# Optimization experiments

Hardware: AMD Instinct MI355X
Metric: run time of the kernel (lower is better)

The kernel has to match this reference:

```python
import jax, jax.numpy as jnp
import numpy as np

H = 128        # num_hidden
NIN = 384      # num_in
FF = 4 * H
SCALE = 30.0
EPS = 1e-5


def _gelu(x):
    return jax.nn.gelu(x, approximate=False)


def _layernorm(x, g, b):
    mu = jnp.mean(x, axis=-1, keepdims=True)
    var = jnp.var(x, axis=-1, keepdims=True)
    return (x - mu) * jax.lax.rsqrt(var + EPS) * g + b


def setup_inputs() -> dict:
    key = jax.random.key(0)
    ks = jax.random.split(key, 12)
    B, N, K = 4, 2048, 48
    s = lambda fan_in: 1.0 / np.sqrt(fan_in)
    inp = {
        "h_V": jax.random.normal(ks[0], (B, N, H), jnp.float32),
        "h_E": jax.random.normal(ks[1], (B, N, K, NIN), jnp.float32),
        "mask_V": jnp.ones((B, N), jnp.float32),
        "mask_attend": jnp.ones((B, N, K), jnp.float32),
        "W1_w": jax.random.uniform(ks[2], (H + NIN, H), jnp.float32, -s(H + NIN), s(H + NIN)),
        "W1_b": jnp.zeros((H,), jnp.float32),
        "W2_w": jax.random.uniform(ks[3], (H, H), jnp.float32, -s(H), s(H)),
        "W2_b": jnp.zeros((H,), jnp.float32),
        "W3_w": jax.random.uniform(ks[4], (H, H), jnp.float32, -s(H), s(H)),
        "W3_b": jnp.zeros((H,), jnp.float32),
        "Win_w": jax.random.uniform(ks[5], (H, FF), jnp.float32, -s(H), s(H)),
        "Win_b": jnp.zeros((FF,), jnp.float32),
        "Wout_w": jax.random.uniform(ks[6], (FF, H), jnp.float32, -s(FF), s(FF)),
        "Wout_b": jnp.zeros((H,), jnp.float32),
        "ln1_g": jnp.ones((H,), jnp.float32),
        "ln1_b": jnp.zeros((H,), jnp.float32),
        "ln2_g": jnp.ones((H,), jnp.float32),
        "ln2_b": jnp.zeros((H,), jnp.float32),
    }
    return inp


def reference(h_V, h_E, mask_V, mask_attend,
              W1_w, W1_b, W2_w, W2_b, W3_w, W3_b,
              Win_w, Win_b, Wout_w, Wout_b,
              ln1_g, ln1_b, ln2_g, ln2_b):
    B, N, K, _ = h_E.shape
    # expand node feats over K neighbors and concat with edge feats -> [B,N,K,H+NIN]
    h_V_expand = jnp.broadcast_to(h_V[:, :, None, :], (B, N, K, h_V.shape[-1]))
    h_EV = jnp.concatenate([h_V_expand, h_E], axis=-1)
    # edge MLP: 3 linears, 2 GELUs
    h_message = _gelu(h_EV @ W1_w + W1_b)
    h_message = _gelu(h_message @ W2_w + W2_b)
    h_message = h_message @ W3_w + W3_b
    h_message = mask_attend[..., None] * h_message
    dh = jnp.sum(h_message, axis=-2) / SCALE  # [B,N,H]
    h = _layernorm(h_V + dh, ln1_g, ln1_b)
    # position-wise FFN
    dh = _gelu(h @ Win_w + Win_b) @ Wout_w + Wout_b
    h = _layernorm(h + dh, ln2_g, ln2_b)
    h = mask_V[..., None] * h
    return h
```

## Files before the change

kernel.cpp:

```cpp
#include <hip/hip_runtime.h>
#include <hip/hip_bf16.h>

#define Hh    128
#define NINc  384
#define KN    48
#define FFd   512
#define NNODE 8192
#define NPB   32
#define EGRID (NNODE/NPB)

typedef __attribute__((ext_vector_type(8))) short short8v;
typedef __attribute__((ext_vector_type(4))) float f32x4;

__device__ __forceinline__ short f2bf1(float f){
  union { __hip_bfloat16 h; short s; } c; c.h = __float2bfloat16(f);
  return c.s;
}
__device__ __forceinline__ unsigned pk_bf16(float lo, float hi){
  union { __hip_bfloat162 h; unsigned u; } c;
  c.h = __float22bfloat162_rn(make_float2(lo, hi));
  return c.u;
}

__device__ __forceinline__ float gelu_f(float x){
  float t = 0.7978845608028654f * x * (1.0f + 0.044715f * x * x);
  float e = __expf(2.0f * t);
  return x * (1.0f - 1.0f / (e + 1.0f));
}

__device__ __forceinline__ void bar_lds(){
  asm volatile("s_waitcnt lgkmcnt(0)\n\ts_barrier" ::: "memory");
}

__global__ void prep_weights(const float* __restrict__ W1, const float* __restrict__ W2,
                             const float* __restrict__ W3, const float* __restrict__ Win,
                             const float* __restrict__ Wout,
                             short* __restrict__ w1vT, short* __restrict__ w1eT,
                             short* __restrict__ w2T,  short* __restrict__ w3T,
                             short* __restrict__ winT, short* __restrict__ woutT)
{
  int i = blockIdx.x * 256 + threadIdx.x;
  if (i < 16384){ int n = i / 128, k = i % 128; w1vT[i] = f2bf1(W1[k*128 + n]); return; }
  i -= 16384;
  if (i < 49152){ int n = i / 384, k = i % 384; w1eT[i] = f2bf1(W1[(128+k)*128 + n]); return; }
  i -= 49152;
  if (i < 16384){ int n = i / 128, k = i % 128; w2T[i] = f2bf1(W2[k*128 + n]); return; }
  i -= 16384;
  if (i < 16384){ int n = i / 128, k = i % 128; w3T[i] = f2bf1(W3[k*128 + n]); return; }
  i -= 16384;
  if (i < 65536){ int n = i / 128, k = i % 128; winT[i] = f2bf1(Win[k*512 + n]); return; }
  i -= 65536;
  if (i < 65536){ int n = i / 512, k = i % 512; woutT[i] = f2bf1(Wout[k*128 + n]); return; }
}

__global__ __launch_bounds__(256,2) void np_kernel(
    const float* __restrict__ hV, const short* __restrict__ w1vT,
    const float* __restrict__ b1, float* __restrict__ npart)
{
  const int row0 = blockIdx.x * 64;
  const int tid = threadIdx.x, lane = tid & 63, wv = tid >> 6;
  __shared__ __attribute__((aligned(16))) short Xs[64][Hh + 8];

  const float4* src = (const float4*)(hV + (size_t)row0 * Hh);
  #pragma unroll
  for (int j = 0; j < 8; ++j){
    int idx = tid + 256*j;
    int r = idx >> 5, c4 = idx & 31;
    float4 v = src[idx];
    unsigned u0 = pk_bf16(v.x, v.y), u1 = pk_bf16(v.z, v.w);
    *(uint2*)&Xs[r][c4*4] = make_uint2(u0, u1);
  }
  __syncthreads();

  const int arow = lane & 15, kgrp = (lane >> 4) * 8;
  const int col0 = wv * 32, ccol = lane & 15, crow0 = (lane >> 4) * 4;

  f32x4 acc[4][2];
  #pragma unroll
  for (int m = 0; m < 4; ++m) for (int n = 0; n < 2; ++n) acc[m][n] = (f32x4){0.f,0.f,0.f,0.f};

  const short8v* Bw = (const short8v*)w1vT;
  #pragma unroll
  for (int ks = 0; ks < 4; ++ks){
    int kb = ks*32 + kgrp;
    short8v b0 = Bw[(col0 + arow)*16      + (kb >> 3)];
    short8v b1f = Bw[(col0 + 16 + arow)*16 + (kb >> 3)];
    #pragma unroll
    for (int m = 0; m < 4; ++m){
      short8v a = *(const short8v*)&Xs[m*16 + arow][kb];
      acc[m][0] = __builtin_amdgcn_mfma_f32_16x16x32_bf16(a, b0,  acc[m][0], 0,0,0);
      acc[m][1] = __builtin_amdgcn_mfma_f32_16x16x32_bf16(a, b1f, acc[m][1], 0,0,0);
    }
  }
  #pragma unroll
  for (int m = 0; m < 4; ++m) for (int n = 0; n < 2; ++n){
    int colg = col0 + n*16 + ccol;
    float bb = b1[colg];
    #pragma unroll
    for (int r = 0; r < 4; ++r)
      npart[(size_t)(row0 + m*16 + crow0 + r)*Hh + colg] = acc[m][n][r] + bb;
  }
}

__global__ __launch_bounds__(512,2) void edge_kernel(
    const float* __restrict__ hE, const float* __restrict__ hV,
    const float* __restrict__ maskA, const float* __restrict__ npart,
    const short* __restrict__ w1eT, const short* __restrict__ w2T,
    const short* __restrict__ w3T,
    const float* __restrict__ b2, const float* __restrict__ b3,
    float* __restrict__ out)
{
  const int tid = threadIdx.x, lane = tid & 63, wv = tid >> 6;
  const int base = blockIdx.x * NPB;

  __shared__ __attribute__((aligned(16))) short Etd[2][KN][NINc + 8];
  __shared__ __attribute__((aligned(16))) short M1[KN][Hh + 8];
  __shared__ __attribute__((aligned(16))) short M2[KN][Hh + 8];
  __shared__ float mskS[2][KN];
  __shared__ float npS[2][Hh], hvS[2][Hh];

  const int arow = lane & 15, kgrp = (lane >> 4) * 8;
  const int ccol = lane & 15, crow0 = (lane >> 4) * 4;
  const int col0 = wv * 16;
  const int colg = col0 + ccol;

  short8v w1f[12], w2f[4], w3f[4];
  {
    const short8v* B1 = (const short8v*)w1eT;
    const short8v* B2 = (const short8v*)w2T;
    const short8v* B3 = (const short8v*)w3T;
    const int rB = col0 + arow;
    #pragma unroll
    for (int ks = 0; ks < 12; ++ks) w1f[ks] = B1[rB*48 + ((ks*32 + kgrp) >> 3)];
    #pragma unroll
    for (int ks = 0; ks < 4; ++ks){
      w2f[ks] = B2[rB*16 + ((ks*32 + kgrp) >> 3)];
      w3f[ks] = B3[rB*16 + ((ks*32 + kgrp) >> 3)];
    }
  }
  const float b2v = b2[colg];
  const float b3v = b3[colg];

  float4 pf[9];
  float  pmsk = 0.f;
  float4 phv  = {0,0,0,0}, pnp = {0,0,0,0};

  auto LOADN = [&](int nn){
    const float4* src = (const float4*)(hE + (size_t)nn * (KN*NINc));
    #pragma unroll
    for (int j = 0; j < 4; ++j){
      pf[2*j]   = src[2*tid + 1024*j];
      pf[2*j+1] = src[2*tid + 1024*j + 1];
    }
    pf[8] = src[4096 + tid];
    if (tid < KN) pmsk = maskA[nn*KN + tid];
    if (tid >= 64 && tid < 96)  phv = *(const float4*)(hV    + (size_t)nn*Hh + (tid-64)*4);
    if (tid >= 96 && tid < 128) pnp = *(const float4*)(npart + (size_t)nn*Hh + (tid-96)*4);
  };
  auto STOREN = [&](int buf){
    #pragma unroll
    for (int j = 0; j < 4; ++j){
      int e0 = 2*tid + 1024*j;
      int r = e0 / 96, c = e0 - r*96;
      uint4 u;
      u.x = pk_bf16(pf[2*j].x,   pf[2*j].y);
      u.y = pk_bf16(pf[2*j].z,   pf[2*j].w);
      u.z = pk_bf16(pf[2*j+1].x, pf[2*j+1].y);
      u.w = pk_bf16(pf[2*j+1].z, pf[2*j+1].w);
      *(uint4*)&Etd[buf][r][c*4] = u;
    }
    { int e = 4096 + tid; int r = e / 96, c = e - r*96;
      *(uint2*)&Etd[buf][r][c*4] =
        make_uint2(pk_bf16(pf[8].x, pf[8].y), pk_bf16(pf[8].z, pf[8].w)); }
    if (tid < KN) mskS[buf][tid] = pmsk;
    if (tid >= 64 && tid < 96)  *(float4*)&hvS[buf][(tid-64)*4] = phv;
    if (tid >= 96 && tid < 128) *(float4*)&npS[buf][(tid-96)*4] = pnp;
  };

  LOADN(base);
  STOREN(0);
  bar_lds();

  int cur = 0;
  for (int t = 0; t < NPB; ++t){
    const int node = base + t;
    if (t + 1 < NPB) LOADN(node + 1);

    {
      f32x4 a1[3];
      #pragma unroll
      for (int m = 0; m < 3; ++m) a1[m] = (f32x4){0.f,0.f,0.f,0.f};
      #pragma unroll
      for (int ks = 0; ks < 12; ++ks){
        int kb = ks*32 + kgrp;
        short8v v0 = *(const short8v*)&Etd[cur][arow][kb];
        short8v v1 = *(const short8v*)&Etd[cur][16 + arow][kb];
        short8v v2 = *(const short8v*)&Etd[cur][32 + arow][kb];
        a1[0] = __builtin_amdgcn_mfma_f32_16x16x32_bf16(v0, w1f[ks], a1[0], 0,0,0);
        a1[1] = __builtin_amdgcn_mfma_f32_16x16x32_bf16(v1, w1f[ks], a1[1], 0,0,0);
        a1[2] = __builtin_amdgcn_mfma_f32_16x16x32_bf16(v2, w1f[ks], a1[2], 0,0,0);
      }
      float npv = npS[cur][colg];
      #pragma unroll
      for (int m = 0; m < 3; ++m)
        #pragma unroll
        for (int r = 0; r < 4; ++r)
          M1[m*16 + crow0 + r][colg] = f2bf1(gelu_f(a1[m][r] + npv));
    }
    bar_lds();

    {
      f32x4 a2[3];
      #pragma unroll
      for (int m = 0; m < 3; ++m) a2[m] = (f32x4){0.f,0.f,0.f,0.f};
      #pragma unroll
      for (int ks = 0; ks < 4; ++ks){
        int kb = ks*32 + kgrp;
        short8v v0 = *(const short8v*)&M1[arow][kb];
        short8v v1 = *(const short8v*)&M1[16 + arow][kb];
        short8v v2 = *(const short8v*)&M1[32 + arow][kb];
        a2[0] = __builtin_amdgcn_mfma_f32_16x16x32_bf16(v0, w2f[ks], a2[0], 0,0,0);
        a2[1] = __builtin_amdgcn_mfma_f32_16x16x32_bf16(v1, w2f[ks], a2[1], 0,0,0);
        a2[2] = __builtin_amdgcn_mfma_f32_16x16x32_bf16(v2, w2f[ks], a2[2], 0,0,0);
      }
      #pragma unroll
      for (int m = 0; m < 3; ++m)
        #pragma unroll
        for (int r = 0; r < 4; ++r)
          M2[m*16 + crow0 + r][colg] = f2bf1(gelu_f(a2[m][r] + b2v));
    }
    bar_lds();

    {
      f32x4 a3[3];
      #pragma unroll
      for (int m = 0; m < 3; ++m) a3[m] = (f32x4){0.f,0.f,0.f,0.f};
      #pragma unroll
      for (int ks = 0; ks < 4; ++ks){
        int kb = ks*32 + kgrp;
        short8v v0 = *(const short8v*)&M2[arow][kb];
        short8v v1 = *(const short8v*)&M2[16 + arow][kb];
        short8v v2 = *(const short8v*)&M2[32 + arow][kb];
        a3[0] = __builtin_amdgcn_mfma_f32_16x16x32_bf16(v0, w3f[ks], a3[0], 0,0,0);
        a3[1] = __builtin_amdgcn_mfma_f32_16x16x32_bf16(v1, w3f[ks], a3[1], 0,0,0);
        a3[2] = __builtin_amdgcn_mfma_f32_16x16x32_bf16(v2, w3f[ks], a3[2], 0,0,0);
      }
      float s = 0.f;
      #pragma unroll
      for (int m = 0; m < 3; ++m)
        #pragma unroll
        for (int r = 0; r < 4; ++r)
          s += (a3[m][r] + b3v) * mskS[cur][m*16 + crow0 + r];
      s += __shfl_xor(s, 16);
      s += __shfl_xor(s, 32);
      if (lane < 16)
        out[(size_t)node*Hh + colg] = hvS[cur][colg] + s * (1.0f/30.0f);
    }

    if (t + 1 < NPB){
      STOREN(cur ^ 1);
      bar_lds();
    }
    cur ^= 1;
  }
}

__global__ __launch_bounds__(256,2) void ffn_kernel(
    const float* __restrict__ ln1g, const float* __restrict__ ln1b,
    const short* __restrict__ winT, const float* __restrict__ bin,
    const short* __restrict__ woutT, const float* __restrict__ bout,
    const float* __restrict__ ln2g, const float* __restrict__ ln2b,
    const float* __restrict__ maskV, float* __restrict__ io)
{
  const int row0 = blockIdx.x * 32;
  const int tid = threadIdx.x, lane = tid & 63, wv = tid >> 6;
  __shared__ __attribute__((aligned(16))) short Xs[32][Hh + 8];
  __shared__ __attribute__((aligned(16))) float Rs[32][Hh + 4];
  __shared__ __attribute__((aligned(16))) short Hs[32][FFd + 8];

  const int arow = lane & 15, kgrp = (lane >> 4) * 8;
  const int ccol = lane & 15, crow0 = (lane >> 4) * 4;

  {
    int r = tid >> 3, cb = (tid & 7) * 16;
    const float4* xp = (const float4*)(io + (size_t)(row0 + r)*Hh + cb);
    float xv[16];
    #pragma unroll
    for (int j = 0; j < 4; ++j){
      float4 v = xp[j];
      xv[j*4+0]=v.x; xv[j*4+1]=v.y; xv[j*4+2]=v.z; xv[j*4+3]=v.w;
    }
    float sum = 0.f, sq = 0.f;
    #pragma unroll
    for (int j = 0; j < 16; ++j){ sum += xv[j]; sq += xv[j]*xv[j]; }
    #pragma unroll
    for (int d = 1; d < 8; d <<= 1){ sum += __shfl_xor(sum, d); sq += __shfl_xor(sq, d); }
    float mu = sum * (1.0f/128.0f);
    float var = sq * (1.0f/128.0f) - mu*mu;
    float rstd = rsqrtf(var + 1e-5f);
    #pragma unroll
    for (int j = 0; j < 16; ++j){
      int c = cb + j;
      float xn = (xv[j] - mu) * rstd * ln1g[c] + ln1b[c];
      Xs[r][c] = f2bf1(xn);
      Rs[r][c] = xn;
    }
  }
  __syncthreads();

  {
    f32x4 acc[2][8];
    #pragma unroll
    for (int m = 0; m < 2; ++m) for (int n = 0; n < 8; ++n) acc[m][n] = (f32x4){0.f,0.f,0.f,0.f};
    const short8v* Bw = (const short8v*)winT;
    #pragma unroll
    for (int ks = 0; ks < 4; ++ks){
      int kb = ks*32 + kgrp;
      short8v a0 = *(const short8v*)&Xs[arow][kb];
      short8v a1 = *(const short8v*)&Xs[16 + arow][kb];
      #pragma unroll
      for (int n = 0; n < 8; ++n){
        short8v b = Bw[(wv*128 + n*16 + arow)*16 + (kb >> 3)];
        acc[0][n] = __builtin_amdgcn_mfma_f32_16x16x32_bf16(a0,b,acc[0][n],0,0,0);
        acc[1][n] = __builtin_amdgcn_mfma_f32_16x16x32_bf16(a1,b,acc[1][n],0,0,0);
      }
    }
    #pragma unroll
    for (int m = 0; m < 2; ++m) for (int n = 0; n < 8; ++n){
      int colg = wv*128 + n*16 + ccol;
      float bb = bin[colg];
      #pragma unroll
      for (int r = 0; r < 4; ++r)
        Hs[m*16 + crow0 + r][colg] = f2bf1(gelu_f(acc[m][n][r] + bb));
    }
  }
  __syncthreads();

  {
    f32x4 acc[2][2];
    #pragma unroll
    for (int m = 0; m < 2; ++m) for (int n = 0; n < 2; ++n) acc[m][n] = (f32x4){0.f,0.f,0.f,0.f};
    const short8v* Bw = (const short8v*)woutT;
    #pragma unroll
    for (int ks = 0; ks < 16; ++ks){
      int kb = ks*32 + kgrp;
      short8v a0 = *(const short8v*)&Hs[arow][kb];
      short8v a1 = *(const short8v*)&Hs[16 + arow][kb];
      short8v b0 = Bw[(wv*32 + arow)*64      + (kb >> 3)];
      short8v b1f = Bw[(wv*32 + 16 + arow)*64 + (kb >> 3)];
      acc[0][0] = __builtin_amdgcn_mfma_f32_16x16x32_bf16(a0,b0, acc[0][0],0,0,0);
      acc[1][0] = __builtin_amdgcn_mfma_f32_16x16x32_bf16(a1,b0, acc[1][0],0,0,0);
      acc[0][1] = __builtin_amdgcn_mfma_f32_16x16x32_bf16(a0,b1f,acc[0][1],0,0,0);
      acc[1][1] = __builtin_amdgcn_mfma_f32_16x16x32_bf16(a1,b1f,acc[1][1],0,0,0);
    }
    #pragma unroll
    for (int m = 0; m < 2; ++m) for (int n = 0; n < 2; ++n){
      int colg = wv*32 + n*16 + ccol;
      float bb = bout[colg];
      #pragma unroll
      for (int r = 0; r < 4; ++r){
        int rr = m*16 + crow0 + r;
        Rs[rr][colg] = Rs[rr][colg] + acc[m][n][r] + bb;
      }
    }
  }
  __syncthreads();

  {
    int r = tid >> 3, cb = (tid & 7) * 16;
    float xv[16];
    #pragma unroll
    for (int j = 0; j < 16; ++j) xv[j] = Rs[r][cb + j];
    float sum = 0.f, sq = 0.f;
    #pragma unroll
    for (int j = 0; j < 16; ++j){ sum += xv[j]; sq += xv[j]*xv[j]; }
    #pragma unroll
    for (int d = 1; d < 8; d <<= 1){ sum += __shfl_xor(sum, d); sq += __shfl_xor(sq, d); }
    float mu = sum * (1.0f/128.0f);
    float var = sq * (1.0f/128.0f) - mu*mu;
    float rstd = rsqrtf(var + 1e-5f);
    float mv = maskV[row0 + r];
    float* op = io + (size_t)(row0 + r)*Hh + cb;
    #pragma unroll
    for (int j = 0; j < 4; ++j){
      float4 o;
      o.x = ((xv[j*4+0] - mu)*rstd*ln2g[cb+j*4+0] + ln2b[cb+j*4+0]) * mv;
      o.y = ((xv[j*4+1] - mu)*rstd*ln2g[cb+j*4+1] + ln2b[cb+j*4+1]) * mv;
      o.z = ((xv[j*4+2] - mu)*rstd*ln2g[cb+j*4+2] + ln2b[cb+j*4+2]) * mv;
      o.w = ((xv[j*4+3] - mu)*rstd*ln2g[cb+j*4+3] + ln2b[cb+j*4+3]) * mv;
      ((float4*)op)[j] = o;
    }
  }
}

extern "C" void kernel_launch(void* const* d_in, const int* in_sizes, int n_in,
                              void* d_out, int out_size, void* d_ws, size_t ws_size,
                              hipStream_t stream)
{
  const float* hV    = (const float*)d_in[0];
  const float* hE    = (const float*)d_in[1];
  const float* maskV = (const float*)d_in[2];
  const float* maskA = (const float*)d_in[3];
  const float* W1w   = (const float*)d_in[4];
  const float* W1b   = (const float*)d_in[5];
  const float* W2w   = (const float*)d_in[6];
  const float* W2b   = (const float*)d_in[7];
  const float* W3w   = (const float*)d_in[8];
  const float* W3b   = (const float*)d_in[9];
  const float* Winw  = (const float*)d_in[10];
  const float* Winb  = (const float*)d_in[11];
  const float* Woutw = (const float*)d_in[12];
  const float* Woutb = (const float*)d_in[13];
  const float* l1g   = (const float*)d_in[14];
  const float* l1b   = (const float*)d_in[15];
  const float* l2g   = (const float*)d_in[16];
  const float* l2b   = (const float*)d_in[17];

  char* ws = (char*)d_ws;
  size_t off = 0;
  float* npart = (float*)(ws + off); off += (size_t)NNODE * Hh * 4;
  short* w1vT  = (short*)(ws + off); off += 128*128*2;
  short* w1eT  = (short*)(ws + off); off += 128*384*2;
  short* w2T   = (short*)(ws + off); off += 128*128*2;
  short* w3T   = (short*)(ws + off); off += 128*128*2;
  short* winT  = (short*)(ws + off); off += 512*128*2;
  short* woutT = (short*)(ws + off); off += 128*512*2;
  if (ws_size < off) return;

  prep_weights<<<896, 256, 0, stream>>>(W1w, W2w, W3w, Winw, Woutw,
                                        w1vT, w1eT, w2T, w3T, winT, woutT);
  np_kernel<<<NNODE/64, 256, 0, stream>>>(hV, w1vT, W1b, npart);
  edge_kernel<<<EGRID, 512, 0, stream>>>(hE, hV, maskA, npart,
                                         w1eT, w2T, w3T, W2b, W3b, (float*)d_out);
  ffn_kernel<<<NNODE/32, 256, 0, stream>>>(l1g, l1b, winT, Winb, woutT, Woutb,
                                           l2g, l2b, maskV, (float*)d_out);
}
```

Before: 225.6 us.

## Restructure edge kernel with staged single-buffer edge loads and lane-swizzled streamed weights

The edge kernel moves from 512 threads with a double-buffered edge tile to 256 threads with one edge tile. The next node's edge rows are loaded in three 16-row slices, each written after the layer that last reads that region, so loads overlap the three MLP layers. Weights are pre-swizzled into per-lane MFMA fragment order and read from global/L2 inside the loops instead of being held in registers. Each wave computes two output column tiles. The M1/M2 scratch buffers are merged and NPB drops to 8 for more blocks. This cuts LDS and register pressure to raise occupancy on the bandwidth-bound edge stream, at the cost of repeated weight fetches and extra barriers.

```diff
diff --git a/kernel.cpp b/kernel.cpp
--- a/kernel.cpp
+++ b/kernel.cpp
@@ -6,7 +6,7 @@
 #define KN    48
 #define FFd   512
 #define NNODE 8192
-#define NPB   32
+#define NPB   8
 #define EGRID (NNODE/NPB)
 
 typedef __attribute__((ext_vector_type(8))) short short8v;
@@ -35,18 +35,36 @@
 __global__ void prep_weights(const float* __restrict__ W1, const float* __restrict__ W2,
                              const float* __restrict__ W3, const float* __restrict__ Win,
                              const float* __restrict__ Wout,
-                             short* __restrict__ w1vT, short* __restrict__ w1eT,
-                             short* __restrict__ w2T,  short* __restrict__ w3T,
+                             short* __restrict__ w1vT, short* __restrict__ w1p,
+                             short* __restrict__ w2p,  short* __restrict__ w3p,
                              short* __restrict__ winT, short* __restrict__ woutT)
 {
   int i = blockIdx.x * 256 + threadIdx.x;
   if (i < 16384){ int n = i / 128, k = i % 128; w1vT[i] = f2bf1(W1[k*128 + n]); return; }
   i -= 16384;
-  if (i < 49152){ int n = i / 384, k = i % 384; w1eT[i] = f2bf1(W1[(128+k)*128 + n]); return; }
+  if (i < 49152){
+    int n = i / 6144, r = i % 6144;
+    int ks = r / 512, r2 = r % 512;
+    int lane = r2 / 8, j = r2 % 8;
+    int qq = lane >> 4, arow = lane & 15;
+    w1p[i] = f2bf1(W1[(128 + ks*32 + qq*8 + j)*128 + n*16 + arow]); return;
+  }
   i -= 49152;
-  if (i < 16384){ int n = i / 128, k = i % 128; w2T[i] = f2bf1(W2[k*128 + n]); return; }
+  if (i < 16384){
+    int n = i / 2048, r = i % 2048;
+    int ks = r / 512, r2 = r % 512;
+    int lane = r2 / 8, j = r2 % 8;
+    int qq = lane >> 4, arow = lane & 15;
+    w2p[i] = f2bf1(W2[(ks*32 + qq*8 + j)*128 + n*16 + arow]); return;
+  }
   i -= 16384;
-  if (i < 16384){ int n = i / 128, k = i % 128; w3T[i] = f2bf1(W3[k*128 + n]); return; }
+  if (i < 16384){
+    int n = i / 2048, r = i % 2048;
+    int ks = r / 512, r2 = r % 512;
+    int lane = r2 / 8, j = r2 % 8;
+    int qq = lane >> 4, arow = lane & 15;
+    w3p[i] = f2bf1(W3[(ks*32 + qq*8 + j)*128 + n*16 + arow]); return;
+  }
   i -= 16384;
   if (i < 65536){ int n = i / 128, k = i % 128; winT[i] = f2bf1(Win[k*512 + n]); return; }
   i -= 65536;
@@ -67,8 +85,7 @@
     int idx = tid + 256*j;
     int r = idx >> 5, c4 = idx & 31;
     float4 v = src[idx];
-    unsigned u0 = pk_bf16(v.x, v.y), u1 = pk_bf16(v.z, v.w);
-    *(uint2*)&Xs[r][c4*4] = make_uint2(u0, u1);
+    *(uint2*)&Xs[r][c4*4] = make_uint2(pk_bf16(v.x,v.y), pk_bf16(v.z,v.w));
   }
   __syncthreads();
 
@@ -102,165 +119,178 @@
   }
 }
 
-__global__ __launch_bounds__(512,2) void edge_kernel(
+__global__ __launch_bounds__(256,3) void edge_kernel(
     const float* __restrict__ hE, const float* __restrict__ hV,
     const float* __restrict__ maskA, const float* __restrict__ npart,
-    const short* __restrict__ w1eT, const short* __restrict__ w2T,
-    const short* __restrict__ w3T,
+    const short* __restrict__ w1p, const short* __restrict__ w2p,
+    const short* __restrict__ w3p,
     const float* __restrict__ b2, const float* __restrict__ b3,
     float* __restrict__ out)
 {
   const int tid = threadIdx.x, lane = tid & 63, wv = tid >> 6;
   const int base = blockIdx.x * NPB;
 
-  __shared__ __attribute__((aligned(16))) short Etd[2][KN][NINc + 8];
-  __shared__ __attribute__((aligned(16))) short M1[KN][Hh + 8];
-  __shared__ __attribute__((aligned(16))) short M2[KN][Hh + 8];
+  __shared__ __attribute__((aligned(16))) short Et[KN][NINc + 8];
+  __shared__ __attribute__((aligned(16))) short M1[KN * 136];
   __shared__ float mskS[2][KN];
   __shared__ float npS[2][Hh], hvS[2][Hh];
 
-  const int arow = lane & 15, kgrp = (lane >> 4) * 8;
-  const int ccol = lane & 15, crow0 = (lane >> 4) * 4;
-  const int col0 = wv * 16;
-  const int colg = col0 + ccol;
-
-  short8v w1f[12], w2f[4], w3f[4];
-  {
-    const short8v* B1 = (const short8v*)w1eT;
-    const short8v* B2 = (const short8v*)w2T;
-    const short8v* B3 = (const short8v*)w3T;
-    const int rB = col0 + arow;
-    #pragma unroll
-    for (int ks = 0; ks < 12; ++ks) w1f[ks] = B1[rB*48 + ((ks*32 + kgrp) >> 3)];
-    #pragma unroll
-    for (int ks = 0; ks < 4; ++ks){
-      w2f[ks] = B2[rB*16 + ((ks*32 + kgrp) >> 3)];
-      w3f[ks] = B3[rB*16 + ((ks*32 + kgrp) >> 3)];
-    }
-  }
-  const float b2v = b2[colg];
-  const float b3v = b3[colg];
-
-  float4 pf[9];
+  const int arow = lane & 15, q = lane >> 4, kgrp = q * 8;
+  const int ccol = lane & 15, crow0 = q * 4;
+  const int n0 = wv*2, n1 = wv*2 + 1;
+  const int colg0 = n0*16 + ccol, colg1 = n1*16 + ccol;
+
+  const float b2v0 = b2[colg0], b2v1 = b2[colg1];
+  const float b3v0 = b3[colg0], b3v1 = b3[colg1];
+
+  const short8v* B1 = (const short8v*)w1p;
+  const short8v* B2 = (const short8v*)w2p;
+  const short8v* B3 = (const short8v*)w3p;
+
+  float4 pf[6];
   float  pmsk = 0.f;
-  float4 phv  = {0,0,0,0}, pnp = {0,0,0,0};
-
-  auto LOADN = [&](int nn){
-    const float4* src = (const float4*)(hE + (size_t)nn * (KN*NINc));
-    #pragma unroll
-    for (int j = 0; j < 4; ++j){
-      pf[2*j]   = src[2*tid + 1024*j];
-      pf[2*j+1] = src[2*tid + 1024*j + 1];
-    }
-    pf[8] = src[4096 + tid];
-    if (tid < KN) pmsk = maskA[nn*KN + tid];
-    if (tid >= 64 && tid < 96)  phv = *(const float4*)(hV    + (size_t)nn*Hh + (tid-64)*4);
-    if (tid >= 96 && tid < 128) pnp = *(const float4*)(npart + (size_t)nn*Hh + (tid-96)*4);
+  float4 phv = {0,0,0,0}, pnp = {0,0,0,0};
+
+  auto LOADT = [&](int nn, int tau){
+    const float4* src = (const float4*)(hE + (size_t)nn * (KN*NINc)) + (32 - 16*tau)*96;
+    #pragma unroll
+    for (int j = 0; j < 6; ++j) pf[j] = src[tid + 256*j];
+    if (tau == 0){
+      if (tid < KN) pmsk = maskA[nn*KN + tid];
+      if (tid >= 64 && tid < 96)  phv = *(const float4*)(hV    + (size_t)nn*Hh + (tid-64)*4);
+      if (tid >= 96 && tid < 128) pnp = *(const float4*)(npart + (size_t)nn*Hh + (tid-96)*4);
+    }
   };
-  auto STOREN = [&](int buf){
-    #pragma unroll
-    for (int j = 0; j < 4; ++j){
-      int e0 = 2*tid + 1024*j;
-      int r = e0 / 96, c = e0 - r*96;
-      uint4 u;
-      u.x = pk_bf16(pf[2*j].x,   pf[2*j].y);
-      u.y = pk_bf16(pf[2*j].z,   pf[2*j].w);
-      u.z = pk_bf16(pf[2*j+1].x, pf[2*j+1].y);
-      u.w = pk_bf16(pf[2*j+1].z, pf[2*j+1].w);
-      *(uint4*)&Etd[buf][r][c*4] = u;
-    }
-    { int e = 4096 + tid; int r = e / 96, c = e - r*96;
-      *(uint2*)&Etd[buf][r][c*4] =
-        make_uint2(pk_bf16(pf[8].x, pf[8].y), pk_bf16(pf[8].z, pf[8].w)); }
-    if (tid < KN) mskS[buf][tid] = pmsk;
-    if (tid >= 64 && tid < 96)  *(float4*)&hvS[buf][(tid-64)*4] = phv;
-    if (tid >= 96 && tid < 128) *(float4*)&npS[buf][(tid-96)*4] = pnp;
+  auto STORET = [&](int tau, int sb){
+    int g = (32 - 16*tau)*96 + tid;
+    #pragma unroll
+    for (int j = 0; j < 6; ++j){
+      int f = g + 256*j;
+      int r = f / 96, c4 = f - r*96;
+      *(uint2*)&Et[r][c4*4] = make_uint2(pk_bf16(pf[j].x, pf[j].y),
+                                         pk_bf16(pf[j].z, pf[j].w));
+    }
+    if (tau == 0){
+      if (tid < KN) mskS[sb][tid] = pmsk;
+      if (tid >= 64 && tid < 96)  *(float4*)&hvS[sb][(tid-64)*4] = phv;
+      if (tid >= 96 && tid < 128) *(float4*)&npS[sb][(tid-96)*4] = pnp;
+    }
   };
 
-  LOADN(base);
-  STOREN(0);
+  LOADT(base, 0); STORET(0, 0);
+  LOADT(base, 1); STORET(1, 0);
+  LOADT(base, 2); STORET(2, 0);
   bar_lds();
 
   int cur = 0;
   for (int t = 0; t < NPB; ++t){
     const int node = base + t;
-    if (t + 1 < NPB) LOADN(node + 1);
-
+    const bool valid = (t + 1 < NPB);
+    if (valid) LOADT(node + 1, 0);
+
+    f32x4 a[3][2];
+    #pragma unroll
+    for (int m = 0; m < 3; ++m) for (int n = 0; n < 2; ++n) a[m][n] = (f32x4){0.f,0.f,0.f,0.f};
+    #pragma unroll
+    for (int ks = 0; ks < 12; ++ks){
+      short8v bA = B1[(n0*12 + ks)*64 + lane];
+      short8v bB = B1[(n1*12 + ks)*64 + lane];
+      int kb = ks*32 + kgrp;
+      short8v v0 = *(const short8v*)&Et[arow][kb];
+      short8v v1 = *(const short8v*)&Et[16 + arow][kb];
+      short8v v2 = *(const short8v*)&Et[32 + arow][kb];
+      a[0][0] = __builtin_amdgcn_mfma_f32_16x16x32_bf16(v0, bA, a[0][0], 0,0,0);
+      a[1][0] = __builtin_amdgcn_mfma_f32_16x16x32_bf16(v1, bA, a[1][0], 0,0,0);
+      a[2][0] = __builtin_amdgcn_mfma_f32_16x16x32_bf16(v2, bA, a[2][0], 0,0,0);
+      a[0][1] = __builtin_amdgcn_mfma_f32_16x16x32_bf16(v0, bB, a[0][1], 0,0,0);
+      a[1][1] = __builtin_amdgcn_mfma_f32_16x16x32_bf16(v1, bB, a[1][1], 0,0,0);
+      a[2][1] = __builtin_amdgcn_mfma_f32_16x16x32_bf16(v2, bB, a[2][1], 0,0,0);
+    }
     {
-      f32x4 a1[3];
-      #pragma unroll
-      for (int m = 0; m < 3; ++m) a1[m] = (f32x4){0.f,0.f,0.f,0.f};
-      #pragma unroll
-      for (int ks = 0; ks < 12; ++ks){
-        int kb = ks*32 + kgrp;
-        short8v v0 = *(const short8v*)&Etd[cur][arow][kb];
-        short8v v1 = *(const short8v*)&Etd[cur][16 + arow][kb];
-        short8v v2 = *(const short8v*)&Etd[cur][32 + arow][kb];
-        a1[0] = __builtin_amdgcn_mfma_f32_16x16x32_bf16(v0, w1f[ks], a1[0], 0,0,0);
-        a1[1] = __builtin_amdgcn_mfma_f32_16x16x32_bf16(v1, w1f[ks], a1[1], 0,0,0);
-        a1[2] = __builtin_amdgcn_mfma_f32_16x16x32_bf16(v2, w1f[ks], a1[2], 0,0,0);
-      }
-      float npv = npS[cur][colg];
+      float npv0 = npS[cur][colg0], npv1 = npS[cur][colg1];
       #pragma unroll
       for (int m = 0; m < 3; ++m)
         #pragma unroll
-        for (int r = 0; r < 4; ++r)
-          M1[m*16 + crow0 + r][colg] = f2bf1(gelu_f(a1[m][r] + npv));
+        for (int r = 0; r < 4; ++r){
+          int row = m*16 + crow0 + r;
+          M1[row*136 + colg0] = f2bf1(gelu_f(a[m][0][r] + npv0));
+          M1[row*136 + colg1] = f2bf1(gelu_f(a[m][1][r] + npv1));
+        }
     }
     bar_lds();
 
+    if (valid){ STORET(0, cur ^ 1); LOADT(node + 1, 1); }
+
+    #pragma unroll
+    for (int m = 0; m < 3; ++m) for (int n = 0; n < 2; ++n) a[m][n] = (f32x4){0.f,0.f,0.f,0.f};
+    #pragma unroll
+    for (int ks = 0; ks < 4; ++ks){
+      short8v bA = B2[(n0*4 + ks)*64 + lane];
+      short8v bB = B2[(n1*4 + ks)*64 + lane];
+      int kb = ks*32 + kgrp;
+      short8v v0 = *(const short8v*)&M1[arow*136 + kb];
+      short8v v1 = *(const short8v*)&M1[(16 + arow)*136 + kb];
+      short8v v2 = *(const short8v*)&M1[(32 + arow)*136 + kb];
+      a[0][0] = __builtin_amdgcn_mfma_f32_16x16x32_bf16(v0, bA, a[0][0], 0,0,0);
+      a[1][0] = __builtin_amdgcn_mfma_f32_16x16x32_bf16(v1, bA, a[1][0], 0,0,0);
+      a[2][0] = __builtin_amdgcn_mfma_f32_16x16x32_bf16(v2, bA, a[2][0], 0,0,0);
+      a[0][1] = __builtin_amdgcn_mfma_f32_16x16x32_bf16(v0, bB, a[0][1], 0,0,0);
+      a[1][1] = __builtin_amdgcn_mfma_f32_16x16x32_bf16(v1, bB, a[1][1], 0,0,0);
+      a[2][1] = __builtin_amdgcn_mfma_f32_16x16x32_bf16(v2, bB, a[2][1], 0,0,0);
+    }
+    bar_lds();
+
+    if (valid){ STORET(1, cur ^ 1); LOADT(node + 1, 2); }
+
     {
-      f32x4 a2[3];
-      #pragma unroll
-      for (int m = 0; m < 3; ++m) a2[m] = (f32x4){0.f,0.f,0.f,0.f};
-      #pragma unroll
-      for (int ks = 0; ks < 4; ++ks){
-        int kb = ks*32 + kgrp;
-        short8v v0 = *(const short8v*)&M1[arow][kb];
-        short8v v1 = *(const short8v*)&M1[16 + arow][kb];
-        short8v v2 = *(const short8v*)&M1[32 + arow][kb];
-        a2[0] = __builtin_amdgcn_mfma_f32_16x16x32_bf16(v0, w2f[ks], a2[0], 0,0,0);
-        a2[1] = __builtin_amdgcn_mfma_f32_16x16x32_bf16(v1, w2f[ks], a2[1], 0,0,0);
-        a2[2] = __builtin_amdgcn_mfma_f32_16x16x32_bf16(v2, w2f[ks], a2[2], 0,0,0);
-      }
       #pragma unroll
       for (int m = 0; m < 3; ++m)
         #pragma unroll
-        for (int r = 0; r < 4; ++r)
-          M2[m*16 + crow0 + r][colg] = f2bf1(gelu_f(a2[m][r] + b2v));
+        for (int r = 0; r < 4; ++r){
+          int row = m*16 + crow0 + r;
+          M1[row*136 + colg0] = f2bf1(gelu_f(a[m][0][r] + b2v0));
+          M1[row*136 + colg1] = f2bf1(gelu_f(a[m][1][r] + b2v1));
+        }
     }
     bar_lds();
 
+    if (valid) STORET(2, cur ^ 1);
+
+    #pragma unroll
+    for (int m = 0; m < 3; ++m) for (int n = 0; n < 2; ++n) a[m][n] = (f32x4){0.f,0.f,0.f,0.f};
+    #pragma unroll
+    for (int ks = 0; ks < 4; ++ks){
+      short8v bA = B3[(n0*4 + ks)*64 + lane];
+      short8v bB = B3[(n1*4 + ks)*64 + lane];
+      int kb = ks*32 + kgrp;
+      short8v v0 = *(const short8v*)&M1[arow*136 + kb];
+      short8v v1 = *(const short8v*)&M1[(16 + arow)*136 + kb];
+      short8v v2 = *(const short8v*)&M1[(32 + arow)*136 + kb];
+      a[0][0] = __builtin_amdgcn_mfma_f32_16x16x32_bf16(v0, bA, a[0][0], 0,0,0);
+      a[1][0] = __builtin_amdgcn_mfma_f32_16x16x32_bf16(v1, bA, a[1][0], 0,0,0);
+      a[2][0] = __builtin_amdgcn_mfma_f32_16x16x32_bf16(v2, bA, a[2][0], 0,0,0);
+      a[0][1] = __builtin_amdgcn_mfma_f32_16x16x32_bf16(v0, bB, a[0][1], 0,0,0);
+      a[1][1] = __builtin_amdgcn_mfma_f32_16x16x32_bf16(v1, bB, a[1][1], 0,0,0);
+      a[2][1] = __builtin_amdgcn_mfma_f32_16x16x32_bf16(v2, bB, a[2][1], 0,0,0);
+    }
     {
-      f32x4 a3[3];
-      #pragma unroll
-      for (int m = 0; m < 3; ++m) a3[m] = (f32x4){0.f,0.f,0.f,0.f};
-      #pragma unroll
-      for (int ks = 0; ks < 4; ++ks){
-        int kb = ks*32 + kgrp;
-        short8v v0 = *(const short8v*)&M2[arow][kb];
-        short8v v1 = *(const short8v*)&M2[16 + arow][kb];
-        short8v v2 = *(const short8v*)&M2[32 + arow][kb];
-        a3[0] = __builtin_amdgcn_mfma_f32_16x16x32_bf16(v0, w3f[ks], a3[0], 0,0,0);
-        a3[1] = __builtin_amdgcn_mfma_f32_16x16x32_bf16(v1, w3f[ks], a3[1], 0,0,0);
-        a3[2] = __builtin_amdgcn_mfma_f32_16x16x32_bf16(v2, w3f[ks], a3[2], 0,0,0);
-      }
-      float s = 0.f;
+      float s0 = 0.f, s1 = 0.f;
       #pragma unroll
       for (int m = 0; m < 3; ++m)
         #pragma unroll
-        for (int r = 0; r < 4; ++r)
-          s += (a3[m][r] + b3v) * mskS[cur][m*16 + crow0 + r];
-      s += __shfl_xor(s, 16);
-      s += __shfl_xor(s, 32);
-      if (lane < 16)
-        out[(size_t)node*Hh + colg] = hvS[cur][colg] + s * (1.0f/30.0f);
-    }
-
-    if (t + 1 < NPB){
-      STOREN(cur ^ 1);
-      bar_lds();
-    }
+        for (int r = 0; r < 4; ++r){
+          float mk = mskS[cur][m*16 + crow0 + r];
+          s0 += (a[m][0][r] + b3v0) * mk;
+          s1 += (a[m][1][r] + b3v1) * mk;
+        }
+      s0 += __shfl_xor(s0, 16); s0 += __shfl_xor(s0, 32);
+      s1 += __shfl_xor(s1, 16); s1 += __shfl_xor(s1, 32);
+      if (lane < 16){
+        out[(size_t)node*Hh + colg0] = hvS[cur][colg0] + s0 * (1.0f/30.0f);
+        out[(size_t)node*Hh + colg1] = hvS[cur][colg1] + s1 * (1.0f/30.0f);
+      }
+    }
+    bar_lds();
     cur ^= 1;
   }
 }
@@ -419,19 +449,19 @@
   char* ws = (char*)d_ws;
   size_t off = 0;
   float* npart = (float*)(ws + off); off += (size_t)NNODE * Hh * 4;
-  short* w1vT  = (short*)(ws + off); off += 128*128*2;
-  short* w1eT  = (short*)(ws + off); off += 128*384*2;
-  short* w2T   = (short*)(ws + off); off += 128*128*2;
-  short* w3T   = (short*)(ws + off); off += 128*128*2;
-  short* winT  = (short*)(ws + off); off += 512*128*2;
-  short* woutT = (short*)(ws + off); off += 128*512*2;
+  short* w1vT  = (short*)(ws + off); off += 16384*2;
+  short* w1p   = (short*)(ws + off); off += 49152*2;
+  short* w2p   = (short*)(ws + off); off += 16384*2;
+  short* w3p   = (short*)(ws + off); off += 16384*2;
+  short* winT  = (short*)(ws + off); off += 65536*2;
+  short* woutT = (short*)(ws + off); off += 65536*2;
   if (ws_size < off) return;
 
   prep_weights<<<896, 256, 0, stream>>>(W1w, W2w, W3w, Winw, Woutw,
-                                        w1vT, w1eT, w2T, w3T, winT, woutT);
+                                        w1vT, w1p, w2p, w3p, winT, woutT);
   np_kernel<<<NNODE/64, 256, 0, stream>>>(hV, w1vT, W1b, npart);
-  edge_kernel<<<EGRID, 512, 0, stream>>>(hE, hV, maskA, npart,
-                                         w1eT, w2T, w3T, W2b, W3b, (float*)d_out);
+  edge_kernel<<<EGRID, 256, 0, stream>>>(hE, hV, maskA, npart,
+                                         w1p, w2p, w3p, W2b, W3b, (float*)d_out);
   ffn_kernel<<<NNODE/32, 256, 0, stream>>>(l1g, l1b, winT, Winb, woutT, Woutb,
                                            l2g, l2b, maskV, (float*)d_out);
 }
```

Measured after the change: 427.4 us. 1.89x slower.
